# Performance work log

Measured on AMD Instinct MI355X. Metric: run time of the kernel, lower is better.

The kernel has to match this reference:

```python
import jax, jax.numpy as jnp
import numpy as np

N_NODES = 100000
N_EDGES = 600000
N_GRAPHS = 512


def _glorot(key, shape):
    fan_in, fan_out = shape
    lim = np.sqrt(6.0 / (fan_in + fan_out)).astype(np.float32)
    return jax.random.uniform(key, shape, jnp.float32, -lim, lim)


def setup_inputs() -> dict:
    key = jax.random.key(0)
    ks = jax.random.split(key, 12)
    x = jax.random.normal(ks[0], (N_NODES, 3), jnp.float32)
    edge_index = jax.random.randint(ks[1], (2, N_EDGES), 0, N_NODES, jnp.int64)
    batch = jnp.sort(jax.random.randint(ks[2], (N_NODES,), 0, N_GRAPHS, jnp.int64))
    return {
        "x": x,
        "edge_index": edge_index,
        "batch": batch,
        "W1": _glorot(ks[3], (3, 128)),   "b1": jnp.zeros((128,), jnp.float32),
        "W2": _glorot(ks[4], (128, 128)), "b2": jnp.zeros((128,), jnp.float32),
        "W3": _glorot(ks[5], (128, 64)),  "b3": jnp.zeros((64,), jnp.float32),
        "Wl": _glorot(ks[6], (64, 1)),    "bl": jnp.zeros((1,), jnp.float32),
    }


def _gcn_conv(h, W, b, src, dst, deg_inv_sqrt):
    # linear transform, then normalized gather-scatter aggregation (self-loops
    # already included in src/dst and deg_inv_sqrt).
    h = h @ W                                            # [N, F_out]
    norm = deg_inv_sqrt[src] * deg_inv_sqrt[dst]         # [E+N]
    msg = h[src] * norm[:, None]                         # [E+N, F_out]
    out = jax.ops.segment_sum(msg, dst, num_segments=N_NODES)
    return out + b


def reference(x, edge_index, batch, W1, b1, W2, b2, W3, b3, Wl, bl):
    # add self-loops (GCNConv default add_self_loops=True)
    loop = jnp.arange(N_NODES, dtype=edge_index.dtype)
    src = jnp.concatenate([edge_index[0], loop])
    dst = jnp.concatenate([edge_index[1], loop])
    # symmetric normalization deg^{-1/2} (in-degree at target, edge weight 1)
    deg = jax.ops.segment_sum(jnp.ones_like(dst, jnp.float32), dst,
                              num_segments=N_NODES)
    deg_inv_sqrt = jnp.where(deg > 0, jax.lax.rsqrt(jnp.maximum(deg, 1.0)), 0.0)

    h = jax.nn.relu(_gcn_conv(x, W1, b1, src, dst, deg_inv_sqrt))
    h = jax.nn.relu(_gcn_conv(h, W2, b2, src, dst, deg_inv_sqrt))
    h = jax.nn.relu(_gcn_conv(h, W3, b3, src, dst, deg_inv_sqrt))

    # global mean pool over graphs
    sums = jax.ops.segment_sum(h, batch, num_segments=N_GRAPHS)    # [G, 64]
    counts = jax.ops.segment_sum(jnp.ones((N_NODES,), jnp.float32), batch,
                                 num_segments=N_GRAPHS)
    pooled = sums / jnp.maximum(counts, 1.0)[:, None]

    return pooled @ Wl + bl                                        # [G, 1]
```

## Files before the change

kernel.cpp:

```cpp
#include <hip/hip_runtime.h>

#define N_NODES 100000
#define N_EDGES 600000
#define N_GRAPHS 512

typedef __attribute__((ext_vector_type(8))) short short8;
typedef __attribute__((ext_vector_type(4))) float floatx4;
typedef __attribute__((ext_vector_type(2))) float floatx2;

__device__ __forceinline__ unsigned short f2bf(float f) {
    unsigned int u = __float_as_uint(f);
    u += 0x7FFFu + ((u >> 16) & 1u);
    return (unsigned short)(u >> 16);
}
__device__ __forceinline__ short8 pack8(const float* a) {
    short8 r;
    #pragma unroll
    for (int j = 0; j < 8; ++j) r[j] = (short)f2bf(a[j]);
    return r;
}

__device__ __forceinline__ uint2 pack_fp8x8(const float* v) {
    uint2 r;
    unsigned int a = 0;
    a = __builtin_amdgcn_cvt_pk_fp8_f32(v[0], v[1], a, 0);
    a = __builtin_amdgcn_cvt_pk_fp8_f32(v[2], v[3], a, 1);
    unsigned int b = 0;
    b = __builtin_amdgcn_cvt_pk_fp8_f32(v[4], v[5], b, 0);
    b = __builtin_amdgcn_cvt_pk_fp8_f32(v[6], v[7], b, 1);
    r.x = a; r.y = b;
    return r;
}
__device__ __forceinline__ unsigned char f2fp8(float v) {
    return (unsigned char)(__builtin_amdgcn_cvt_pk_fp8_f32(v, v, 0u, 0) & 0xFFu);
}
__device__ __forceinline__ void fma4_fp8(float* a, unsigned int w, float n) {
    floatx2 p;
    p = __builtin_amdgcn_cvt_pk_f32_fp8(w, 0); a[0] = fmaf(p[0], n, a[0]); a[1] = fmaf(p[1], n, a[1]);
    p = __builtin_amdgcn_cvt_pk_f32_fp8(w, 1); a[2] = fmaf(p[0], n, a[2]); a[3] = fmaf(p[1], n, a[3]);
}
__device__ __forceinline__ void init4_fp8(float* a, unsigned int w, float s) {
    floatx2 p;
    p = __builtin_amdgcn_cvt_pk_f32_fp8(w, 0); a[0] = p[0] * s; a[1] = p[1] * s;
    p = __builtin_amdgcn_cvt_pk_f32_fp8(w, 1); a[2] = p[0] * s; a[3] = p[1] * s;
}
__device__ __forceinline__ void fma16_fp8(float* a, uint4 v, float n) {
    fma4_fp8(a +  0, v.x, n); fma4_fp8(a +  4, v.y, n);
    fma4_fp8(a +  8, v.z, n); fma4_fp8(a + 12, v.w, n);
}
__device__ __forceinline__ void init16_fp8(float* a, uint4 v, float s) {
    init4_fp8(a +  0, v.x, s); init4_fp8(a +  4, v.y, s);
    init4_fp8(a +  8, v.z, s); init4_fp8(a + 12, v.w, s);
}

__global__ void k_hist(const int* __restrict__ dst, int* cnt) {
    int e = blockIdx.x * 256 + threadIdx.x;
    if (e < N_EDGES) atomicAdd(&cnt[dst[e]], 1);
}

__global__ void k_scan1(const int* __restrict__ cnt, int* __restrict__ part) {
    __shared__ int s[256];
    int t = threadIdx.x;
    int i = blockIdx.x * 256 + t;
    int v = (i < N_NODES) ? cnt[i] : 0;
    s[t] = v; __syncthreads();
    for (int off = 128; off > 0; off >>= 1) {
        if (t < off) s[t] += s[t + off];
        __syncthreads();
    }
    if (t == 0) part[blockIdx.x] = s[0];
}

__global__ void k_scan3(const int* __restrict__ cnt, const int* __restrict__ part,
                        int* __restrict__ row_ptr, int* __restrict__ cursor,
                        float* __restrict__ dis) {
    __shared__ int s[256];
    __shared__ int pbaseS;
    int t = threadIdx.x;
    int psum = 0;
    for (int k = t; k < blockIdx.x; k += 256) psum += part[k];
    s[t] = psum; __syncthreads();
    for (int off = 128; off > 0; off >>= 1) {
        if (t < off) s[t] += s[t + off];
        __syncthreads();
    }
    if (t == 0) pbaseS = s[0];
    __syncthreads();
    int pbase = pbaseS;
    __syncthreads();
    int i = blockIdx.x * 256 + t;
    int v = (i < N_NODES) ? cnt[i] : 0;
    s[t] = v; __syncthreads();
    for (int off = 1; off < 256; off <<= 1) {
        int u = (t >= off) ? s[t - off] : 0;
        __syncthreads();
        s[t] += u;
        __syncthreads();
    }
    int ex = s[t] - v + pbase;
    if (i < N_NODES) {
        row_ptr[i] = ex; cursor[i] = ex;
        dis[i] = 1.0f / sqrtf((float)(v + 1));
    }
    if (blockIdx.x == 0 && t == 0) row_ptr[N_NODES] = N_EDGES;
}

__global__ void k_scatter(const int* __restrict__ src, const int* __restrict__ dst,
                          const float* __restrict__ dis, int* __restrict__ cursor,
                          int* __restrict__ csr_src, float* __restrict__ csr_norm) {
    int e = blockIdx.x * 256 + threadIdx.x;
    if (e >= N_EDGES) return;
    int s = src[e], d = dst[e];
    int pos = atomicAdd(&cursor[d], 1);
    csr_src[pos] = s;
    csr_norm[pos] = dis[s] * dis[d];
}

__device__ __forceinline__ void pack_one(const float* __restrict__ W, unsigned short* __restrict__ out,
                                         int idx, int N) {
    int lane = idx & 63;
    int ks = (idx >> 6) & 3;
    int ct = idx >> 8;
    int n = ct * 16 + (lane & 15);
    int kbase = ks * 32 + (lane >> 4) * 8;
    #pragma unroll
    for (int j = 0; j < 8; ++j)
        out[(size_t)idx * 8 + j] = f2bf(W[(size_t)(kbase + j) * N + n]);
}

#define NB1 6250
__global__ __launch_bounds__(256) void k_node1(const float* __restrict__ x,
                                               const float* __restrict__ dis,
                                               const int* __restrict__ row_ptr,
                                               const int* __restrict__ csr_src,
                                               const float* __restrict__ csr_norm,
                                               const float* __restrict__ W1,
                                               const float* __restrict__ b1,
                                               unsigned char* __restrict__ out,
                                               const float* __restrict__ W2,
                                               const float* __restrict__ W3,
                                               unsigned short* __restrict__ Wp2,
                                               unsigned short* __restrict__ Wp3) {
    int tid = threadIdx.x;
    if (blockIdx.x >= NB1) {
        int idx = (blockIdx.x - NB1) * 256 + tid;
        if (idx < 2048) pack_one(W2, Wp2, idx, 128);
        else if (idx < 3072) pack_one(W3, Wp3, idx - 2048, 64);
        return;
    }
    __shared__ float Ws[384];
    __shared__ float bs[128];
    for (int i = tid; i < 384; i += 256) Ws[i] = W1[i];
    if (tid < 128) bs[tid] = b1[tid];
    __syncthreads();
    int gw = (blockIdx.x * 256 + tid) >> 6;
    int lane = tid & 63;
    int sub = lane >> 4, l16 = lane & 15;
    int node = gw * 4 + sub;
    int beg = row_ptr[node], end = row_ptr[node + 1];
    float p0 = 0.f, p1 = 0.f, p2 = 0.f;
    for (int e = beg + l16; e < end; e += 16) {
        int s = csr_src[e];
        float n = csr_norm[e];
        p0 = fmaf(x[s * 3 + 0], n, p0);
        p1 = fmaf(x[s * 3 + 1], n, p1);
        p2 = fmaf(x[s * 3 + 2], n, p2);
    }
    #pragma unroll
    for (int m = 8; m > 0; m >>= 1) {
        p0 += __shfl_xor(p0, m, 64);
        p1 += __shfl_xor(p1, m, 64);
        p2 += __shfl_xor(p2, m, 64);
    }
    float d = dis[node], s2 = d * d;
    float a0 = fmaf(x[node * 3 + 0], s2, p0);
    float a1 = fmaf(x[node * 3 + 1], s2, p1);
    float a2 = fmaf(x[node * 3 + 2], s2, p2);
    int f = l16 * 8;
    float v[8];
    #pragma unroll
    for (int j = 0; j < 8; ++j)
        v[j] = fmaxf(bs[f + j] + a0 * Ws[f + j] + a1 * Ws[128 + f + j] + a2 * Ws[256 + f + j], 0.f);
    *(uint2*)(out + (size_t)node * 128 + f) = pack_fp8x8(v);
}

__global__ __launch_bounds__(256) void k_layer23(const unsigned char* __restrict__ h1,
                                                 const float* __restrict__ dis,
                                                 const int* __restrict__ row_ptr,
                                                 const int* __restrict__ csr_src,
                                                 const float* __restrict__ csr_norm,
                                                 const unsigned short* __restrict__ Wp2,
                                                 const float* __restrict__ b2,
                                                 const unsigned short* __restrict__ Wp3,
                                                 unsigned char* __restrict__ Q2f8) {
    __shared__ unsigned short Asb[32][136];
    __shared__ unsigned short Hsb[32][136];
    int tid = threadIdx.x;
    int wave = tid >> 6, lane = tid & 63;
    int quad = lane >> 4, m16 = lane & 15;
    int base = blockIdx.x * 32;

    {
        int sub = lane >> 3, l8 = lane & 7;
        int r = wave * 8 + sub;
        int node = base + r;
        int beg = row_ptr[node], end = row_ptr[node + 1];
        int idx[8]; float nn[8];
        #pragma unroll
        for (int u = 0; u < 8; ++u) {
            int ee = beg + u; int cl = ee < end ? ee : end - 1;
            idx[u] = csr_src[cl]; nn[u] = ee < end ? csr_norm[cl] : 0.0f;
        }
        float d = dis[node];
        uint4 self = *(const uint4*)(h1 + (size_t)node * 128 + l8 * 16);
        uint4 g[8];
        #pragma unroll
        for (int u = 0; u < 8; ++u)
            g[u] = *(const uint4*)(h1 + (size_t)idx[u] * 128 + l8 * 16);
        float a[16];
        init16_fp8(a, self, d * d);
        #pragma unroll
        for (int u = 0; u < 8; ++u) fma16_fp8(a, g[u], nn[u]);
        for (int e = beg + 8; e < end; e += 8) {
            int idx2[8]; float nn2[8];
            #pragma unroll
            for (int u = 0; u < 8; ++u) {
                int ee = e + u; int cl = ee < end ? ee : end - 1;
                idx2[u] = csr_src[cl]; nn2[u] = ee < end ? csr_norm[cl] : 0.0f;
            }
            uint4 g2[8];
            #pragma unroll
            for (int u = 0; u < 8; ++u)
                g2[u] = *(const uint4*)(h1 + (size_t)idx2[u] * 128 + l8 * 16);
            #pragma unroll
            for (int u = 0; u < 8; ++u) fma16_fp8(a, g2[u], nn2[u]);
        }
        *(short8*)(&Asb[r][l8 * 16])     = pack8(a);
        *(short8*)(&Asb[r][l8 * 16 + 8]) = pack8(a + 8);
    }
    __syncthreads();

    int mt = wave & 1;
    int ch = wave >> 1;
    {
        short8 af[4];
        #pragma unroll
        for (int ks = 0; ks < 4; ++ks)
            af[ks] = *(const short8*)(&Asb[mt * 16 + m16][ks * 32 + quad * 8]);
        floatx4 acc[4];
        #pragma unroll
        for (int ct = 0; ct < 4; ++ct) acc[ct] = (floatx4){0.f, 0.f, 0.f, 0.f};
        #pragma unroll
        for (int ct = 0; ct < 4; ++ct) {
            int gct = ch * 4 + ct;
            #pragma unroll
            for (int ks = 0; ks < 4; ++ks) {
                short8 bf = *(const short8*)(Wp2 + ((size_t)(gct * 4 + ks) * 64 + lane) * 8);
                acc[ct] = __builtin_amdgcn_mfma_f32_16x16x32_bf16(af[ks], bf, acc[ct], 0, 0, 0);
            }
        }
        #pragma unroll
        for (int ct = 0; ct < 4; ++ct) {
            int col = (ch * 4 + ct) * 16 + m16;
            float bv = b2[col];
            #pragma unroll
            for (int r = 0; r < 4; ++r) {
                int row = mt * 16 + quad * 4 + r;
                Hsb[row][col] = f2bf(fmaxf(acc[ct][r] + bv, 0.0f));
            }
        }
    }
    __syncthreads();

    {
        int cp = wave >> 1;
        short8 hf[4];
        #pragma unroll
        for (int ks = 0; ks < 4; ++ks)
            hf[ks] = *(const short8*)(&Hsb[mt * 16 + m16][ks * 32 + quad * 8]);
        floatx4 acc3[2];
        acc3[0] = (floatx4){0.f, 0.f, 0.f, 0.f};
        acc3[1] = (floatx4){0.f, 0.f, 0.f, 0.f};
        #pragma unroll
        for (int ct = 0; ct < 2; ++ct) {
            int gct = cp * 2 + ct;
            #pragma unroll
            for (int ks = 0; ks < 4; ++ks) {
                short8 bf = *(const short8*)(Wp3 + ((size_t)(gct * 4 + ks) * 64 + lane) * 8);
                acc3[ct] = __builtin_amdgcn_mfma_f32_16x16x32_bf16(hf[ks], bf, acc3[ct], 0, 0, 0);
            }
        }
        #pragma unroll
        for (int ct = 0; ct < 2; ++ct) {
            int col = (cp * 2 + ct) * 16 + m16;
            #pragma unroll
            for (int r = 0; r < 4; ++r) {
                long row = base + mt * 16 + quad * 4 + r;
                Q2f8[row * 64 + col] = f2fp8(acc3[ct][r]);
            }
        }
    }
}

__global__ __launch_bounds__(256) void k_agg64_dot(const unsigned char* __restrict__ h,
                                                   const float* __restrict__ dis,
                                                   const int* __restrict__ row_ptr,
                                                   const int* __restrict__ csr_src,
                                                   const float* __restrict__ csr_norm,
                                                   const float* __restrict__ bias,
                                                   const float* __restrict__ Wl,
                                                   float* __restrict__ s_out) {
    int gw = (blockIdx.x * 256 + threadIdx.x) >> 6;
    if (gw >= N_NODES / 16) return;
    int lane = threadIdx.x & 63;
    int sub = lane >> 2, l4 = lane & 3;
    int node = gw * 16 + sub;
    int beg = row_ptr[node], end = row_ptr[node + 1];
    int idx[8]; float nn[8];
    #pragma unroll
    for (int u = 0; u < 8; ++u) {
        int ee = beg + u; int cl = ee < end ? ee : end - 1;
        idx[u] = csr_src[cl]; nn[u] = ee < end ? csr_norm[cl] : 0.0f;
    }
    float d = dis[node];
    uint4 self = *(const uint4*)(h + (size_t)node * 64 + l4 * 16);
    uint4 g[8];
    #pragma unroll
    for (int u = 0; u < 8; ++u)
        g[u] = *(const uint4*)(h + (size_t)idx[u] * 64 + l4 * 16);
    float a[16];
    init16_fp8(a, self, d * d);
    #pragma unroll
    for (int u = 0; u < 8; ++u) fma16_fp8(a, g[u], nn[u]);
    for (int e = beg + 8; e < end; e += 8) {
        int idx2[8]; float nn2[8];
        #pragma unroll
        for (int u = 0; u < 8; ++u) {
            int ee = e + u; int cl = ee < end ? ee : end - 1;
            idx2[u] = csr_src[cl]; nn2[u] = ee < end ? csr_norm[cl] : 0.0f;
        }
        uint4 g2[8];
        #pragma unroll
        for (int u = 0; u < 8; ++u)
            g2[u] = *(const uint4*)(h + (size_t)idx2[u] * 64 + l4 * 16);
        #pragma unroll
        for (int u = 0; u < 8; ++u) fma16_fp8(a, g2[u], nn2[u]);
    }
    int f = l4 * 16;
    float v = 0.f;
    #pragma unroll
    for (int j = 0; j < 16; ++j)
        v = fmaf(fmaxf(a[j] + bias[f + j], 0.f), Wl[f + j], v);
    v += __shfl_xor(v, 1, 64);
    v += __shfl_xor(v, 2, 64);
    if (l4 == 0) s_out[node] = v;
}

__global__ __launch_bounds__(256) void k_pool2(const float* __restrict__ s,
                                               const int* __restrict__ batch,
                                               const float* __restrict__ bl,
                                               float* __restrict__ out) {
    int g = blockIdx.x;
    int tid = threadIdx.x;
    int lo = 0, hi = N_NODES;
    while (lo < hi) { int m = (lo + hi) >> 1; if (batch[m] < g) lo = m + 1; else hi = m; }
    int lo2 = lo, hi2 = N_NODES;
    while (lo2 < hi2) { int m = (lo2 + hi2) >> 1; if (batch[m] < g + 1) lo2 = m + 1; else hi2 = m; }
    float acc = 0.0f;
    for (int n = lo + tid; n < lo2; n += 256) acc += s[n];
    __shared__ float sm[256];
    sm[tid] = acc; __syncthreads();
    for (int off = 128; off > 0; off >>= 1) {
        if (tid < off) sm[tid] += sm[tid + off];
        __syncthreads();
    }
    if (tid == 0) out[g] = sm[0] / fmaxf((float)(lo2 - lo), 1.0f) + bl[0];
}

extern "C" void kernel_launch(void* const* d_in, const int* in_sizes, int n_in,
                              void* d_out, int out_size, void* d_ws, size_t ws_size,
                              hipStream_t stream) {
    const float* x     = (const float*)d_in[0];
    const int*   ei    = (const int*)d_in[1];
    const int*   batch = (const int*)d_in[2];
    const float* W1 = (const float*)d_in[3];
    const float* b1 = (const float*)d_in[4];
    const float* W2 = (const float*)d_in[5];
    const float* b2 = (const float*)d_in[6];
    const float* W3 = (const float*)d_in[7];
    const float* b3 = (const float*)d_in[8];
    const float* Wl = (const float*)d_in[9];
    const float* bl = (const float*)d_in[10];
    float* out = (float*)d_out;

    const int* e_src = ei;
    const int* e_dst = ei + N_EDGES;

    char* ws = (char*)d_ws;
    size_t off = 0;
    auto alloc = [&](size_t bytes) -> char* {
        char* p = ws + off;
        off = (off + bytes + 255) & ~(size_t)255;
        return p;
    };
    int*   cnt      = (int*)  alloc((size_t)N_NODES * 4);
    float* dis      = (float*)alloc((size_t)N_NODES * 4);
    int*   row_ptr  = (int*)  alloc((size_t)(N_NODES + 1) * 4);
    int*   cursor   = (int*)  alloc((size_t)N_NODES * 4);
    int*   part     = (int*)  alloc(1024 * 4);
    int*   csr_src  = (int*)  alloc((size_t)N_EDGES * 4);
    float* csr_norm = (float*)alloc((size_t)N_EDGES * 4);
    float* nscal    = (float*)alloc((size_t)N_NODES * 4);
    unsigned char*  P1f8 = (unsigned char*) alloc((size_t)N_NODES * 128);
    unsigned char*  Q2f8 = (unsigned char*) alloc((size_t)N_NODES * 64);
    unsigned short* Wp2  = (unsigned short*)alloc((size_t)128 * 128 * 2);
    unsigned short* Wp3  = (unsigned short*)alloc((size_t)128 * 64 * 2);

    const int NB_N = (N_NODES + 255) / 256;
    const int NB_E = (N_EDGES + 255) / 256;

    hipMemsetAsync(cnt, 0, (size_t)N_NODES * 4, stream);
    k_hist<<<NB_E, 256, 0, stream>>>(e_dst, cnt);
    k_scan1<<<NB_N, 256, 0, stream>>>(cnt, part);
    k_scan3<<<NB_N, 256, 0, stream>>>(cnt, part, row_ptr, cursor, dis);
    k_scatter<<<NB_E, 256, 0, stream>>>(e_src, e_dst, dis, cursor, csr_src, csr_norm);

    k_node1<<<NB1 + 12, 256, 0, stream>>>(x, dis, row_ptr, csr_src, csr_norm,
                                          W1, b1, P1f8, W2, W3, Wp2, Wp3);

    k_layer23<<<N_NODES / 32, 256, 0, stream>>>(P1f8, dis, row_ptr, csr_src, csr_norm,
                                                Wp2, b2, Wp3, Q2f8);

    k_agg64_dot<<<(N_NODES / 16 + 3) / 4, 256, 0, stream>>>(Q2f8, dis, row_ptr, csr_src, csr_norm,
                                                            b3, Wl, nscal);

    k_pool2<<<N_GRAPHS, 256, 0, stream>>>(nscal, batch, bl, out);
}
```

Before: 203.4 us.

## Fuse whole GCN pipeline into one cooperative persistent kernel with grid syncs

Replaces the sequence of eight kernel launches plus a memset with a single cooperative kernel that runs every stage (histogram, scan, CSR scatter, layer 1, layers 2-3, layer-3 aggregation, pooling) in grid-stride loops separated by grid.sync(). The goal is to remove launch overhead and inter-kernel gaps. The scan is redone so each block sums all preceding counts directly, which is quadratic-ish work, and stages now run on a capped grid of at most 1024 blocks. The original multi-kernel path is kept as a fallback if the cooperative launch fails.

Result: slower. 735.0 us (+261.4%).

```diff
diff --git a/kernel.cpp b/kernel.cpp
--- a/kernel.cpp
+++ b/kernel.cpp
@@ -1,4 +1,7 @@
 #include <hip/hip_runtime.h>
+#include <hip/hip_cooperative_groups.h>
+
+namespace cg = cooperative_groups;
 
 #define N_NODES 100000
 #define N_EDGES 600000
@@ -51,6 +54,318 @@
 __device__ __forceinline__ void init16_fp8(float* a, uint4 v, float s) {
     init4_fp8(a +  0, v.x, s); init4_fp8(a +  4, v.y, s);
     init4_fp8(a +  8, v.z, s); init4_fp8(a + 12, v.w, s);
+}
+
+__device__ __forceinline__ void pack_one(const float* __restrict__ W, unsigned short* __restrict__ out,
+                                         int idx, int N) {
+    int lane = idx & 63;
+    int ks = (idx >> 6) & 3;
+    int ct = idx >> 8;
+    int n = ct * 16 + (lane & 15);
+    int kbase = ks * 32 + (lane >> 4) * 8;
+    #pragma unroll
+    for (int j = 0; j < 8; ++j)
+        out[(size_t)idx * 8 + j] = f2bf(W[(size_t)(kbase + j) * N + n]);
+}
+
+union alignas(16) SMem {
+    struct { int s[256]; int pbase; } scan;
+    struct { float Ws[384]; float bs[128]; } n1;
+    struct { unsigned short Asb[32][136]; unsigned short Hsb[32][136]; } l23;
+    float pool[256];
+};
+
+__global__ __launch_bounds__(256, 4) void k_mega(
+    const float* __restrict__ x,
+    const int* __restrict__ e_src, const int* __restrict__ e_dst,
+    const int* __restrict__ batch,
+    const float* __restrict__ W1, const float* __restrict__ b1,
+    const float* __restrict__ W2, const float* __restrict__ b2,
+    const float* __restrict__ W3, const float* __restrict__ b3,
+    const float* __restrict__ Wl, const float* __restrict__ bl,
+    float* __restrict__ out,
+    int* __restrict__ cnt, float* __restrict__ dis,
+    int* __restrict__ row_ptr, int* __restrict__ cursor,
+    int* __restrict__ csr_src, float* __restrict__ csr_norm,
+    float* __restrict__ nscal,
+    unsigned char* __restrict__ P1f8, unsigned char* __restrict__ Q2f8,
+    unsigned short* __restrict__ Wp2, unsigned short* __restrict__ Wp3)
+{
+    cg::grid_group grid = cg::this_grid();
+    __shared__ SMem sm;
+
+    const int tid = threadIdx.x;
+    const int nb  = gridDim.x;
+    const int gsz = nb * 256;
+    const int g0  = blockIdx.x * 256 + tid;
+
+    for (int i = g0; i < N_NODES; i += gsz) cnt[i] = 0;
+    for (int idx = g0; idx < 3072; idx += gsz) {
+        if (idx < 2048) pack_one(W2, Wp2, idx, 128);
+        else            pack_one(W3, Wp3, idx - 2048, 64);
+    }
+    grid.sync();
+
+    for (int e = g0; e < N_EDGES; e += gsz) atomicAdd(&cnt[e_dst[e]], 1);
+    grid.sync();
+
+    {
+        const int NSB = (N_NODES + 255) / 256;
+        for (int vb = blockIdx.x; vb < NSB; vb += nb) {
+            int psum = 0;
+            const int lim = vb * 256;
+            for (int k = tid; k < lim; k += 256) psum += cnt[k];
+            sm.scan.s[tid] = psum; __syncthreads();
+            for (int off = 128; off > 0; off >>= 1) {
+                if (tid < off) sm.scan.s[tid] += sm.scan.s[tid + off];
+                __syncthreads();
+            }
+            if (tid == 0) sm.scan.pbase = sm.scan.s[0];
+            __syncthreads();
+            int pbase = sm.scan.pbase;
+            __syncthreads();
+            int i = vb * 256 + tid;
+            int v = (i < N_NODES) ? cnt[i] : 0;
+            sm.scan.s[tid] = v; __syncthreads();
+            for (int off = 1; off < 256; off <<= 1) {
+                int u = (tid >= off) ? sm.scan.s[tid - off] : 0;
+                __syncthreads();
+                sm.scan.s[tid] += u;
+                __syncthreads();
+            }
+            int ex = sm.scan.s[tid] - v + pbase;
+            if (i < N_NODES) {
+                row_ptr[i] = ex; cursor[i] = ex;
+                dis[i] = 1.0f / sqrtf((float)(v + 1));
+            }
+            if (vb == 0 && tid == 0) row_ptr[N_NODES] = N_EDGES;
+            __syncthreads();
+        }
+    }
+    grid.sync();
+
+    for (int e = g0; e < N_EDGES; e += gsz) {
+        int s = e_src[e], d = e_dst[e];
+        int pos = atomicAdd(&cursor[d], 1);
+        csr_src[pos] = s;
+        csr_norm[pos] = dis[s] * dis[d];
+    }
+    grid.sync();
+
+    {
+        for (int i = tid; i < 384; i += 256) sm.n1.Ws[i] = W1[i];
+        if (tid < 128) sm.n1.bs[tid] = b1[tid];
+        __syncthreads();
+        const int wv = tid >> 6;
+        const int lane = tid & 63;
+        const int sub = lane >> 4, l16 = lane & 15;
+        for (int vb = blockIdx.x; vb < N_NODES / 16; vb += nb) {
+            int gw = vb * 4 + wv;
+            int node = gw * 4 + sub;
+            int beg = row_ptr[node], end = row_ptr[node + 1];
+            float p0 = 0.f, p1 = 0.f, p2 = 0.f;
+            for (int e = beg + l16; e < end; e += 16) {
+                int s = csr_src[e];
+                float n = csr_norm[e];
+                p0 = fmaf(x[s * 3 + 0], n, p0);
+                p1 = fmaf(x[s * 3 + 1], n, p1);
+                p2 = fmaf(x[s * 3 + 2], n, p2);
+            }
+            #pragma unroll
+            for (int m = 8; m > 0; m >>= 1) {
+                p0 += __shfl_xor(p0, m, 64);
+                p1 += __shfl_xor(p1, m, 64);
+                p2 += __shfl_xor(p2, m, 64);
+            }
+            float d = dis[node], s2 = d * d;
+            float a0 = fmaf(x[node * 3 + 0], s2, p0);
+            float a1 = fmaf(x[node * 3 + 1], s2, p1);
+            float a2 = fmaf(x[node * 3 + 2], s2, p2);
+            int f = l16 * 8;
+            float v[8];
+            #pragma unroll
+            for (int j = 0; j < 8; ++j)
+                v[j] = fmaxf(sm.n1.bs[f + j] + a0 * sm.n1.Ws[f + j]
+                             + a1 * sm.n1.Ws[128 + f + j] + a2 * sm.n1.Ws[256 + f + j], 0.f);
+            *(uint2*)(P1f8 + (size_t)node * 128 + f) = pack_fp8x8(v);
+        }
+    }
+    grid.sync();
+
+    {
+        const int wv = tid >> 6, lane = tid & 63;
+        const int quad = lane >> 4, m16 = lane & 15;
+        for (int vt = blockIdx.x; vt < N_NODES / 32; vt += nb) {
+            int base = vt * 32;
+
+            {
+                int sub = lane >> 3, l8 = lane & 7;
+                int r = wv * 8 + sub;
+                int node = base + r;
+                int beg = row_ptr[node], end = row_ptr[node + 1];
+                int idx[8]; float nn[8];
+                #pragma unroll
+                for (int u = 0; u < 8; ++u) {
+                    int ee = beg + u; int cl = ee < end ? ee : end - 1;
+                    idx[u] = csr_src[cl]; nn[u] = ee < end ? csr_norm[cl] : 0.0f;
+                }
+                float d = dis[node];
+                uint4 self = *(const uint4*)(P1f8 + (size_t)node * 128 + l8 * 16);
+                uint4 g[8];
+                #pragma unroll
+                for (int u = 0; u < 8; ++u)
+                    g[u] = *(const uint4*)(P1f8 + (size_t)idx[u] * 128 + l8 * 16);
+                float a[16];
+                init16_fp8(a, self, d * d);
+                #pragma unroll
+                for (int u = 0; u < 8; ++u) fma16_fp8(a, g[u], nn[u]);
+                for (int e = beg + 8; e < end; e += 8) {
+                    int idx2[8]; float nn2[8];
+                    #pragma unroll
+                    for (int u = 0; u < 8; ++u) {
+                        int ee = e + u; int cl = ee < end ? ee : end - 1;
+                        idx2[u] = csr_src[cl]; nn2[u] = ee < end ? csr_norm[cl] : 0.0f;
+                    }
+                    uint4 g2[8];
+                    #pragma unroll
+                    for (int u = 0; u < 8; ++u)
+                        g2[u] = *(const uint4*)(P1f8 + (size_t)idx2[u] * 128 + l8 * 16);
+                    #pragma unroll
+                    for (int u = 0; u < 8; ++u) fma16_fp8(a, g2[u], nn2[u]);
+                }
+                *(short8*)(&sm.l23.Asb[r][l8 * 16])     = pack8(a);
+                *(short8*)(&sm.l23.Asb[r][l8 * 16 + 8]) = pack8(a + 8);
+            }
+            __syncthreads();
+
+            int mt = wv & 1;
+            int ch = wv >> 1;
+            {
+                short8 af[4];
+                #pragma unroll
+                for (int ks = 0; ks < 4; ++ks)
+                    af[ks] = *(const short8*)(&sm.l23.Asb[mt * 16 + m16][ks * 32 + quad * 8]);
+                floatx4 acc[4];
+                #pragma unroll
+                for (int ct = 0; ct < 4; ++ct) acc[ct] = (floatx4){0.f, 0.f, 0.f, 0.f};
+                #pragma unroll
+                for (int ct = 0; ct < 4; ++ct) {
+                    int gct = ch * 4 + ct;
+                    #pragma unroll
+                    for (int ks = 0; ks < 4; ++ks) {
+                        short8 bf = *(const short8*)(Wp2 + ((size_t)(gct * 4 + ks) * 64 + lane) * 8);
+                        acc[ct] = __builtin_amdgcn_mfma_f32_16x16x32_bf16(af[ks], bf, acc[ct], 0, 0, 0);
+                    }
+                }
+                #pragma unroll
+                for (int ct = 0; ct < 4; ++ct) {
+                    int col = (ch * 4 + ct) * 16 + m16;
+                    float bv = b2[col];
+                    #pragma unroll
+                    for (int r = 0; r < 4; ++r) {
+                        int row = mt * 16 + quad * 4 + r;
+                        sm.l23.Hsb[row][col] = f2bf(fmaxf(acc[ct][r] + bv, 0.0f));
+                    }
+                }
+            }
+            __syncthreads();
+
+            {
+                int cp = wv >> 1;
+                short8 hf[4];
+                #pragma unroll
+                for (int ks = 0; ks < 4; ++ks)
+                    hf[ks] = *(const short8*)(&sm.l23.Hsb[mt * 16 + m16][ks * 32 + quad * 8]);
+                floatx4 acc3[2];
+                acc3[0] = (floatx4){0.f, 0.f, 0.f, 0.f};
+                acc3[1] = (floatx4){0.f, 0.f, 0.f, 0.f};
+                #pragma unroll
+                for (int ct = 0; ct < 2; ++ct) {
+                    int gct = cp * 2 + ct;
+                    #pragma unroll
+                    for (int ks = 0; ks < 4; ++ks) {
+                        short8 bf = *(const short8*)(Wp3 + ((size_t)(gct * 4 + ks) * 64 + lane) * 8);
+                        acc3[ct] = __builtin_amdgcn_mfma_f32_16x16x32_bf16(hf[ks], bf, acc3[ct], 0, 0, 0);
+                    }
+                }
+                #pragma unroll
+                for (int ct = 0; ct < 2; ++ct) {
+                    int col = (cp * 2 + ct) * 16 + m16;
+                    #pragma unroll
+                    for (int r = 0; r < 4; ++r) {
+                        long row = base + mt * 16 + quad * 4 + r;
+                        Q2f8[row * 64 + col] = f2fp8(acc3[ct][r]);
+                    }
+                }
+            }
+            __syncthreads();
+        }
+    }
+    grid.sync();
+
+    {
+        const int wv = tid >> 6, lane = tid & 63;
+        const int sub = lane >> 2, l4 = lane & 3;
+        for (int vw = blockIdx.x * 4 + wv; vw < N_NODES / 16; vw += nb * 4) {
+            int node = vw * 16 + sub;
+            int beg = row_ptr[node], end = row_ptr[node + 1];
+            int idx[8]; float nn[8];
+            #pragma unroll
+            for (int u = 0; u < 8; ++u) {
+                int ee = beg + u; int cl = ee < end ? ee : end - 1;
+                idx[u] = csr_src[cl]; nn[u] = ee < end ? csr_norm[cl] : 0.0f;
+            }
+            float d = dis[node];
+            uint4 self = *(const uint4*)(Q2f8 + (size_t)node * 64 + l4 * 16);
+            uint4 g[8];
+            #pragma unroll
+            for (int u = 0; u < 8; ++u)
+                g[u] = *(const uint4*)(Q2f8 + (size_t)idx[u] * 64 + l4 * 16);
+            float a[16];
+            init16_fp8(a, self, d * d);
+            #pragma unroll
+            for (int u = 0; u < 8; ++u) fma16_fp8(a, g[u], nn[u]);
+            for (int e = beg + 8; e < end; e += 8) {
+                int idx2[8]; float nn2[8];
+                #pragma unroll
+                for (int u = 0; u < 8; ++u) {
+                    int ee = e + u; int cl = ee < end ? ee : end - 1;
+                    idx2[u] = csr_src[cl]; nn2[u] = ee < end ? csr_norm[cl] : 0.0f;
+                }
+                uint4 g2[8];
+                #pragma unroll
+                for (int u = 0; u < 8; ++u)
+                    g2[u] = *(const uint4*)(Q2f8 + (size_t)idx2[u] * 64 + l4 * 16);
+                #pragma unroll
+                for (int u = 0; u < 8; ++u) fma16_fp8(a, g2[u], nn2[u]);
+            }
+            int f = l4 * 16;
+            float v = 0.f;
+            #pragma unroll
+            for (int j = 0; j < 16; ++j)
+                v = fmaf(fmaxf(a[j] + b3[f + j], 0.f), Wl[f + j], v);
+            v += __shfl_xor(v, 1, 64);
+            v += __shfl_xor(v, 2, 64);
+            if (l4 == 0) nscal[node] = v;
+        }
+    }
+    grid.sync();
+
+    for (int g = blockIdx.x; g < N_GRAPHS; g += nb) {
+        int lo = 0, hi = N_NODES;
+        while (lo < hi) { int m = (lo + hi) >> 1; if (batch[m] < g) lo = m + 1; else hi = m; }
+        int lo2 = lo, hi2 = N_NODES;
+        while (lo2 < hi2) { int m = (lo2 + hi2) >> 1; if (batch[m] < g + 1) lo2 = m + 1; else hi2 = m; }
+        float acc = 0.0f;
+        for (int n = lo + tid; n < lo2; n += 256) acc += nscal[n];
+        sm.pool[tid] = acc; __syncthreads();
+        for (int off = 128; off > 0; off >>= 1) {
+            if (tid < off) sm.pool[tid] += sm.pool[tid + off];
+            __syncthreads();
+        }
+        if (tid == 0) out[g] = sm.pool[0] / fmaxf((float)(lo2 - lo), 1.0f) + bl[0];
+        __syncthreads();
+    }
 }
 
 __global__ void k_hist(const int* __restrict__ dst, int* cnt) {
@@ -114,18 +429,6 @@
     int pos = atomicAdd(&cursor[d], 1);
     csr_src[pos] = s;
     csr_norm[pos] = dis[s] * dis[d];
-}
-
-__device__ __forceinline__ void pack_one(const float* __restrict__ W, unsigned short* __restrict__ out,
-                                         int idx, int N) {
-    int lane = idx & 63;
-    int ks = (idx >> 6) & 3;
-    int ct = idx >> 8;
-    int n = ct * 16 + (lane & 15);
-    int kbase = ks * 32 + (lane >> 4) * 8;
-    #pragma unroll
-    for (int j = 0; j < 8; ++j)
-        out[(size_t)idx * 8 + j] = f2bf(W[(size_t)(kbase + j) * N + n]);
 }
 
 #define NB1 6250
@@ -199,7 +502,6 @@
     int wave = tid >> 6, lane = tid & 63;
     int quad = lane >> 4, m16 = lane & 15;
     int base = blockIdx.x * 32;
-
     {
         int sub = lane >> 3, l8 = lane & 7;
         int r = wave * 8 + sub;
@@ -239,7 +541,6 @@
         *(short8*)(&Asb[r][l8 * 16 + 8]) = pack8(a + 8);
     }
     __syncthreads();
-
     int mt = wave & 1;
     int ch = wave >> 1;
     {
@@ -271,7 +572,6 @@
         }
     }
     __syncthreads();
-
     {
         int cp = wave >> 1;
         short8 hf[4];
@@ -416,6 +716,24 @@
     unsigned short* Wp2  = (unsigned short*)alloc((size_t)128 * 128 * 2);
     unsigned short* Wp3  = (unsigned short*)alloc((size_t)128 * 64 * 2);
 
+    int occ = 0;
+    if (hipOccupancyMaxActiveBlocksPerMultiprocessor(&occ, k_mega, 256, 0) != hipSuccess || occ <= 0)
+        occ = 4;
+    int grid = occ * 256;
+    if (grid > 1024) grid = 1024;
+
+    void* args[] = { (void*)&x, (void*)&e_src, (void*)&e_dst, (void*)&batch,
+                     (void*)&W1, (void*)&b1, (void*)&W2, (void*)&b2,
+                     (void*)&W3, (void*)&b3, (void*)&Wl, (void*)&bl,
+                     (void*)&out,
+                     (void*)&cnt, (void*)&dis, (void*)&row_ptr, (void*)&cursor,
+                     (void*)&csr_src, (void*)&csr_norm, (void*)&nscal,
+                     (void*)&P1f8, (void*)&Q2f8, (void*)&Wp2, (void*)&Wp3 };
+
+    hipError_t err = hipLaunchCooperativeKernel(k_mega, dim3(grid), dim3(256),
+                                                args, 0, stream);
+    if (err == hipSuccess) return;
+
     const int NB_N = (N_NODES + 255) / 256;
     const int NB_E = (N_EDGES + 255) / 256;
 
@@ -424,15 +742,11 @@
     k_scan1<<<NB_N, 256, 0, stream>>>(cnt, part);
     k_scan3<<<NB_N, 256, 0, stream>>>(cnt, part, row_ptr, cursor, dis);
     k_scatter<<<NB_E, 256, 0, stream>>>(e_src, e_dst, dis, cursor, csr_src, csr_norm);
-
     k_node1<<<NB1 + 12, 256, 0, stream>>>(x, dis, row_ptr, csr_src, csr_norm,
                                           W1, b1, P1f8, W2, W3, Wp2, Wp3);
-
     k_layer23<<<N_NODES / 32, 256, 0, stream>>>(P1f8, dis, row_ptr, csr_src, csr_norm,
                                                 Wp2, b2, Wp3, Q2f8);
-
     k_agg64_dot<<<(N_NODES / 16 + 3) / 4, 256, 0, stream>>>(Q2f8, dis, row_ptr, csr_src, csr_norm,
                                                             b3, Wl, nscal);
-
     k_pool2<<<N_GRAPHS, 256, 0, stream>>>(nscal, batch, bl, out);
 }
```

## Merge scan passes, fold pooling into atomics, move weight packing to hist

Applied to the files above, without the earlier changes.

The two-pass scan becomes a single kernel in which each block sums all preceding counts directly, which removes the partial-sum kernel and one launch. The per-node scalar buffer and the per-graph pooling reduction kernel are replaced by atomicAdd into per-graph sums inside the last aggregation kernel, followed by a tiny finalize kernel. Weight packing moves from the node1 kernel into the histogram kernel. The trade-offs are redundant reads of cnt in later scan blocks, atomic contention on 512 graph slots, and non-deterministic float summation order.

Measured after the change: 369.2 us. 1.82x slower.

```diff
diff --git a/kernel.cpp b/kernel.cpp
--- a/kernel.cpp
+++ b/kernel.cpp
@@ -53,32 +53,42 @@
     init4_fp8(a +  8, v.z, s); init4_fp8(a + 12, v.w, s);
 }
 
-__global__ void k_hist(const int* __restrict__ dst, int* cnt) {
+__device__ __forceinline__ void pack_one(const float* __restrict__ W, unsigned short* __restrict__ out,
+                                         int idx, int N) {
+    int lane = idx & 63;
+    int ks = (idx >> 6) & 3;
+    int ct = idx >> 8;
+    int n = ct * 16 + (lane & 15);
+    int kbase = ks * 32 + (lane >> 4) * 8;
+    #pragma unroll
+    for (int j = 0; j < 8; ++j)
+        out[(size_t)idx * 8 + j] = f2bf(W[(size_t)(kbase + j) * N + n]);
+}
+
+#define NB_E ((N_EDGES + 255) / 256)
+__global__ void k_hist_pack(const int* __restrict__ dst, int* cnt,
+                            const float* __restrict__ W2, const float* __restrict__ W3,
+                            unsigned short* __restrict__ Wp2, unsigned short* __restrict__ Wp3) {
+    if (blockIdx.x >= NB_E) {
+        int idx = (blockIdx.x - NB_E) * 256 + threadIdx.x;
+        if (idx < 2048) pack_one(W2, Wp2, idx, 128);
+        else if (idx < 3072) pack_one(W3, Wp3, idx - 2048, 64);
+        return;
+    }
     int e = blockIdx.x * 256 + threadIdx.x;
     if (e < N_EDGES) atomicAdd(&cnt[dst[e]], 1);
 }
 
-__global__ void k_scan1(const int* __restrict__ cnt, int* __restrict__ part) {
-    __shared__ int s[256];
-    int t = threadIdx.x;
-    int i = blockIdx.x * 256 + t;
-    int v = (i < N_NODES) ? cnt[i] : 0;
-    s[t] = v; __syncthreads();
-    for (int off = 128; off > 0; off >>= 1) {
-        if (t < off) s[t] += s[t + off];
-        __syncthreads();
-    }
-    if (t == 0) part[blockIdx.x] = s[0];
-}
-
-__global__ void k_scan3(const int* __restrict__ cnt, const int* __restrict__ part,
-                        int* __restrict__ row_ptr, int* __restrict__ cursor,
-                        float* __restrict__ dis) {
+__global__ void k_scan(const int* __restrict__ cnt,
+                       int* __restrict__ row_ptr, int* __restrict__ cursor,
+                       float* __restrict__ dis, float* __restrict__ gsum) {
     __shared__ int s[256];
     __shared__ int pbaseS;
     int t = threadIdx.x;
+    if (blockIdx.x == 0) { gsum[t] = 0.0f; gsum[t + 256] = 0.0f; }
     int psum = 0;
-    for (int k = t; k < blockIdx.x; k += 256) psum += part[k];
+    const int lim = blockIdx.x * 256;
+    for (int k = t; k < lim; k += 256) psum += cnt[k];
     s[t] = psum; __syncthreads();
     for (int off = 128; off > 0; off >>= 1) {
         if (t < off) s[t] += s[t + off];
@@ -116,18 +126,6 @@
     csr_norm[pos] = dis[s] * dis[d];
 }
 
-__device__ __forceinline__ void pack_one(const float* __restrict__ W, unsigned short* __restrict__ out,
-                                         int idx, int N) {
-    int lane = idx & 63;
-    int ks = (idx >> 6) & 3;
-    int ct = idx >> 8;
-    int n = ct * 16 + (lane & 15);
-    int kbase = ks * 32 + (lane >> 4) * 8;
-    #pragma unroll
-    for (int j = 0; j < 8; ++j)
-        out[(size_t)idx * 8 + j] = f2bf(W[(size_t)(kbase + j) * N + n]);
-}
-
 #define NB1 6250
 __global__ __launch_bounds__(256) void k_node1(const float* __restrict__ x,
                                                const float* __restrict__ dis,
@@ -136,18 +134,8 @@
                                                const float* __restrict__ csr_norm,
                                                const float* __restrict__ W1,
                                                const float* __restrict__ b1,
-                                               unsigned char* __restrict__ out,
-                                               const float* __restrict__ W2,
-                                               const float* __restrict__ W3,
-                                               unsigned short* __restrict__ Wp2,
-                                               unsigned short* __restrict__ Wp3) {
+                                               unsigned char* __restrict__ out) {
     int tid = threadIdx.x;
-    if (blockIdx.x >= NB1) {
-        int idx = (blockIdx.x - NB1) * 256 + tid;
-        if (idx < 2048) pack_one(W2, Wp2, idx, 128);
-        else if (idx < 3072) pack_one(W3, Wp3, idx - 2048, 64);
-        return;
-    }
     __shared__ float Ws[384];
     __shared__ float bs[128];
     for (int i = tid; i < 384; i += 256) Ws[i] = W1[i];
@@ -309,7 +297,8 @@
                                                    const float* __restrict__ csr_norm,
                                                    const float* __restrict__ bias,
                                                    const float* __restrict__ Wl,
-                                                   float* __restrict__ s_out) {
+                                                   const int* __restrict__ batch,
+                                                   float* __restrict__ gsum) {
     int gw = (blockIdx.x * 256 + threadIdx.x) >> 6;
     if (gw >= N_NODES / 16) return;
     int lane = threadIdx.x & 63;
@@ -353,28 +342,19 @@
         v = fmaf(fmaxf(a[j] + bias[f + j], 0.f), Wl[f + j], v);
     v += __shfl_xor(v, 1, 64);
     v += __shfl_xor(v, 2, 64);
-    if (l4 == 0) s_out[node] = v;
-}
-
-__global__ __launch_bounds__(256) void k_pool2(const float* __restrict__ s,
-                                               const int* __restrict__ batch,
-                                               const float* __restrict__ bl,
-                                               float* __restrict__ out) {
-    int g = blockIdx.x;
-    int tid = threadIdx.x;
+    if (l4 == 0) atomicAdd(&gsum[batch[node]], v);
+}
+
+__global__ void k_poolfin(const float* __restrict__ gsum,
+                          const int* __restrict__ batch,
+                          const float* __restrict__ bl,
+                          float* __restrict__ out) {
+    int g = threadIdx.x;
     int lo = 0, hi = N_NODES;
     while (lo < hi) { int m = (lo + hi) >> 1; if (batch[m] < g) lo = m + 1; else hi = m; }
     int lo2 = lo, hi2 = N_NODES;
     while (lo2 < hi2) { int m = (lo2 + hi2) >> 1; if (batch[m] < g + 1) lo2 = m + 1; else hi2 = m; }
-    float acc = 0.0f;
-    for (int n = lo + tid; n < lo2; n += 256) acc += s[n];
-    __shared__ float sm[256];
-    sm[tid] = acc; __syncthreads();
-    for (int off = 128; off > 0; off >>= 1) {
-        if (tid < off) sm[tid] += sm[tid + off];
-        __syncthreads();
-    }
-    if (tid == 0) out[g] = sm[0] / fmaxf((float)(lo2 - lo), 1.0f) + bl[0];
+    out[g] = gsum[g] / fmaxf((float)(lo2 - lo), 1.0f) + bl[0];
 }
 
 extern "C" void kernel_launch(void* const* d_in, const int* in_sizes, int n_in,
@@ -407,32 +387,31 @@
     float* dis      = (float*)alloc((size_t)N_NODES * 4);
     int*   row_ptr  = (int*)  alloc((size_t)(N_NODES + 1) * 4);
     int*   cursor   = (int*)  alloc((size_t)N_NODES * 4);
-    int*   part     = (int*)  alloc(1024 * 4);
+    float* gsum     = (float*)alloc((size_t)N_GRAPHS * 4);
     int*   csr_src  = (int*)  alloc((size_t)N_EDGES * 4);
     float* csr_norm = (float*)alloc((size_t)N_EDGES * 4);
-    float* nscal    = (float*)alloc((size_t)N_NODES * 4);
     unsigned char*  P1f8 = (unsigned char*) alloc((size_t)N_NODES * 128);
     unsigned char*  Q2f8 = (unsigned char*) alloc((size_t)N_NODES * 64);
     unsigned short* Wp2  = (unsigned short*)alloc((size_t)128 * 128 * 2);
     unsigned short* Wp3  = (unsigned short*)alloc((size_t)128 * 64 * 2);
 
     const int NB_N = (N_NODES + 255) / 256;
-    const int NB_E = (N_EDGES + 255) / 256;
 
     hipMemsetAsync(cnt, 0, (size_t)N_NODES * 4, stream);
-    k_hist<<<NB_E, 256, 0, stream>>>(e_dst, cnt);
-    k_scan1<<<NB_N, 256, 0, stream>>>(cnt, part);
-    k_scan3<<<NB_N, 256, 0, stream>>>(cnt, part, row_ptr, cursor, dis);
+
+    k_hist_pack<<<NB_E + 12, 256, 0, stream>>>(e_dst, cnt, W2, W3, Wp2, Wp3);
+
+    k_scan<<<NB_N, 256, 0, stream>>>(cnt, row_ptr, cursor, dis, gsum);
+
     k_scatter<<<NB_E, 256, 0, stream>>>(e_src, e_dst, dis, cursor, csr_src, csr_norm);
 
-    k_node1<<<NB1 + 12, 256, 0, stream>>>(x, dis, row_ptr, csr_src, csr_norm,
-                                          W1, b1, P1f8, W2, W3, Wp2, Wp3);
+    k_node1<<<NB1, 256, 0, stream>>>(x, dis, row_ptr, csr_src, csr_norm, W1, b1, P1f8);
 
     k_layer23<<<N_NODES / 32, 256, 0, stream>>>(P1f8, dis, row_ptr, csr_src, csr_norm,
                                                 Wp2, b2, Wp3, Q2f8);
 
     k_agg64_dot<<<(N_NODES / 16 + 3) / 4, 256, 0, stream>>>(Q2f8, dis, row_ptr, csr_src, csr_norm,
-                                                            b3, Wl, nscal);
-
-    k_pool2<<<N_GRAPHS, 256, 0, stream>>>(nscal, batch, bl, out);
-}
+                                                            b3, Wl, batch, gsum);
+
+    k_poolfin<<<1, N_GRAPHS, 0, stream>>>(gsum, batch, bl, out);
+}
```
